# Kernel tuning notes

Hardware: AMD Instinct MI355X
Metric: run time of the kernel (lower is better)

## Reference

```python
import jax, jax.numpy as jnp
import numpy as np

B, S, D, H, DH, DI, K = 2, 2048, 1024, 16, 64, 4096, 3


def layernorm(x, g, b, eps=1e-5):
    m = x.mean(-1, keepdims=True)
    v = ((x - m) ** 2).mean(-1, keepdims=True)
    return (x - m) * jax.lax.rsqrt(v + eps) * g + b


def setup_inputs() -> dict:
    key = jax.random.key(0)
    ks = jax.random.split(key, 8)
    w = lambda k, shape: jax.random.normal(k, shape, jnp.float32) * 0.02
    return dict(
        dec_inp=jax.random.normal(ks[0], (B, S, D), jnp.float32),
        mask=jnp.ones((B, S, 1), dtype=bool),
        Wq=w(ks[1], (D, H * DH)), bq=jnp.zeros((H * DH,), jnp.float32),
        Wk=w(ks[2], (D, H * DH)), bk=jnp.zeros((H * DH,), jnp.float32),
        Wv=w(ks[3], (D, H * DH)), bv=jnp.zeros((H * DH,), jnp.float32),
        Wo=w(ks[4], (H * DH, D)),
        ln1_g=jnp.ones((D,), jnp.float32), ln1_b=jnp.zeros((D,), jnp.float32),
        conv1_w=w(ks[5], (DI, D, K)), conv1_b=jnp.zeros((DI,), jnp.float32),
        conv2_w=w(ks[6], (D, DI, K)), conv2_b=jnp.zeros((D,), jnp.float32),
        ln2_g=jnp.ones((D,), jnp.float32), ln2_b=jnp.zeros((D,), jnp.float32),
    )


def reference(dec_inp, mask, Wq, bq, Wk, bk, Wv, bv, Wo, ln1_g, ln1_b,
              conv1_w, conv1_b, conv2_w, conv2_b, ln2_g, ln2_b):
    scale = 1.0 / np.sqrt(DH)
    x = dec_inp
    pad = ~mask[:, :, 0]  # [B,S] True = masked-out key position (~mask in torch)
    # QKV projections -> [B,H,S,DH]
    q = (x @ Wq + bq).reshape(B, S, H, DH).transpose(0, 2, 1, 3)
    k = (x @ Wk + bk).reshape(B, S, H, DH).transpose(0, 2, 1, 3)
    v = (x @ Wv + bv).reshape(B, S, H, DH).transpose(0, 2, 1, 3)
    scores = jnp.einsum('bhqd,bhkd->bhqk', q, k) * scale  # [B,H,S,S]
    scores = jnp.where(pad[:, None, None, :], jnp.float32(-100000.0), scores)
    p = jax.nn.softmax(scores, axis=-1)
    av = jnp.einsum('bhqk,bhkd->bhqd', p, v)  # [B,H,S,DH]
    # Replicate torch's view quirk: flat (B*H) reinterpreted as (H,B).
    av = av.reshape(B * H, S, DH).reshape(H, B, S, DH).transpose(1, 2, 0, 3).reshape(B, S, H * DH)
    attn_out = av @ Wo  # o_net has no bias
    out = layernorm(x + attn_out, ln1_g, ln1_b)  # post-lnorm (pre_lnorm=False)
    out = out * mask.astype(out.dtype)
    # Conv FFN (non-causal, 'same' padding)
    h = out.transpose(0, 2, 1)  # [B,D,S] NCH
    pd = K // 2
    dn = ('NCH', 'OIH', 'NCH')
    h1 = jax.lax.conv_general_dilated(h, conv1_w, (1,), [(pd, pd)], dimension_numbers=dn)
    h1 = jax.nn.relu(h1 + conv1_b[None, :, None])
    h2 = jax.lax.conv_general_dilated(h1, conv2_w, (1,), [(pd, pd)], dimension_numbers=dn)
    h2 = h2 + conv2_b[None, :, None]
    out2 = layernorm(out + h2.transpose(0, 2, 1), ln2_g, ln2_b)
    return out2 * mask.astype(out2.dtype)
```

## Files before the change

kernel.cpp:

```cpp
#include <hip/hip_runtime.h>


typedef unsigned short u16;
typedef __attribute__((ext_vector_type(8))) short bf16x8;
typedef __attribute__((ext_vector_type(4))) float f32x4;

__device__ __forceinline__ float us2f(u16 u) {
    return __uint_as_float(((unsigned int)u) << 16);
}
__device__ __forceinline__ u16 f2us(float f) {
    unsigned int i = __float_as_uint(f);
    return (u16)((i + 0x7fffu + ((i >> 16) & 1u)) >> 16);
}
__device__ __forceinline__ f32x4 mfma16(bf16x8 a, bf16x8 b, f32x4 c) {
    return __builtin_amdgcn_mfma_f32_16x16x32_bf16(a, b, c, 0, 0, 0);
}
__device__ __forceinline__ void gld16(const u16* g, u16* l) {
    __builtin_amdgcn_global_load_lds(
        (const __attribute__((address_space(1))) unsigned int*)g,
        (__attribute__((address_space(3))) unsigned int*)l, 16, 0, 0);
}

__global__ __launch_bounds__(64)
void sniff_kernel(const u16* __restrict__ w, int* __restrict__ flag) {
    int t = threadIdx.x;
    u16 v = w[2 * t];
    int e = (v >> 7) & 0xFF;
    int ok = (e >= 100 && e <= 140) ? 1 : 0;
    unsigned long long m = __ballot(ok);
    if (t == 0) *flag = (__popcll(m) < 32) ? 1 : 0;
}

__global__ __launch_bounds__(256)
void cvt_x(const void* __restrict__ src, u16* __restrict__ dst,
           const int* __restrict__ flagp) {
    int idx = (blockIdx.x * 256 + threadIdx.x) * 4;
    if (*flagp) {
        float4 f = *(const float4*)((const float*)src + idx);
        u16 o[4] = {f2us(f.x), f2us(f.y), f2us(f.z), f2us(f.w)};
        *(uint2*)(dst + idx) = *(uint2*)o;
    } else {
        *(uint2*)(dst + idx) = *(const uint2*)((const u16*)src + idx);
    }
}

__global__ __launch_bounds__(256)
void cvt_res(const u16* __restrict__ src, float* __restrict__ dst) {
    int idx = (blockIdx.x * 256 + threadIdx.x) * 4;
    u16 s[4];
    *(uint2*)s = *(const uint2*)(src + idx);
    float4 o = {us2f(s[0]), us2f(s[1]), us2f(s[2]), us2f(s[3])};
    *(float4*)(dst + idx) = o;
}

struct Params9 {
    const void* s[9];
    int n[9];
    int off[9];
};
__global__ __launch_bounds__(256)
void cvt_params(Params9 p, u16* __restrict__ base, const int* __restrict__ flagp) {
    int f = *flagp;
    for (int j = 0; j < 9; ++j) {
        const void* s = p.s[j];
        u16* d = base + p.off[j];
        for (int i = threadIdx.x; i < p.n[j]; i += 256)
            d[i] = f ? f2us(((const float*)s)[i]) : ((const u16*)s)[i];
    }
}

__global__ __launch_bounds__(256)
void transpose4f(const void* s0, const void* s1, const void* s2, const void* s3,
                 u16* __restrict__ d0, u16* __restrict__ d1,
                 u16* __restrict__ d2, u16* __restrict__ d3,
                 const int* __restrict__ flagp) {
    const void* src; u16* dst;
    switch (blockIdx.z) {
        case 0: src = s0; dst = d0; break;
        case 1: src = s1; dst = d1; break;
        case 2: src = s2; dst = d2; break;
        default: src = s3; dst = d3; break;
    }
    int f = *flagp;
    __shared__ u16 tl[32][33];
    int tx = threadIdx.x & 31, ty = threadIdx.x >> 5;
    int xc = blockIdx.x * 32 + tx;
#pragma unroll
    for (int r = 0; r < 4; ++r) {
        int yr = blockIdx.y * 32 + ty + r * 8;
        size_t ix = (size_t)yr * 1024 + xc;
        tl[ty + r * 8][tx] = f ? f2us(((const float*)src)[ix]) : ((const u16*)src)[ix];
    }
    __syncthreads();
    int xc2 = blockIdx.y * 32 + tx;
#pragma unroll
    for (int r = 0; r < 4; ++r) {
        int yr2 = blockIdx.x * 32 + ty + r * 8;
        dst[(size_t)yr2 * 1024 + xc2] = tl[tx][ty + r * 8];
    }
}

__global__ __launch_bounds__(256)
void vtrans(const u16* __restrict__ vb, u16* __restrict__ vtg) {
    __shared__ u16 tl[32][33];
    const int st = blockIdx.x, dt = blockIdx.y, bh = blockIdx.z;
    const int b = bh >> 4, h = bh & 15;
    int tx = threadIdx.x & 31, ty = threadIdx.x >> 5;
#pragma unroll
    for (int r = 0; r < 4; ++r) {
        int s = st * 32 + ty + r * 8;
        tl[ty + r * 8][tx] = vb[(size_t)(b * 2048 + s) * 1024 + h * 64 + dt * 32 + tx];
    }
    __syncthreads();
#pragma unroll
    for (int r = 0; r < 4; ++r) {
        int dh = dt * 32 + ty + r * 8;
        vtg[((size_t)bh * 64 + dh) * 2048 + st * 32 + tx] = tl[tx][ty + r * 8];
    }
}

__global__ __launch_bounds__(256)
void deint3g(const void* __restrict__ src, u16* __restrict__ dst,
             size_t eoff, int rs, int c8b, size_t tstr,
             const int* __restrict__ flagp) {
    int idx = blockIdx.x * 256 + threadIdx.x;
    int row = idx >> c8b;
    int c8 = idx & ((1 << c8b) - 1);
    int C = 8 << c8b;
    u16 e[24];
    if (*flagp) {
        const float* sp = (const float*)src + eoff + (size_t)row * rs + (size_t)c8 * 24;
        float tf[24];
#pragma unroll
        for (int i = 0; i < 6; ++i) *(float4*)(tf + i * 4) = *(const float4*)(sp + i * 4);
#pragma unroll
        for (int i = 0; i < 24; ++i) e[i] = f2us(tf[i]);
    } else {
        const u16* sp = (const u16*)src + eoff + (size_t)row * rs + (size_t)c8 * 24;
        *(uint4*)(e + 0)  = *(const uint4*)(sp + 0);
        *(uint4*)(e + 8)  = *(const uint4*)(sp + 8);
        *(uint4*)(e + 16) = *(const uint4*)(sp + 16);
    }
#pragma unroll
    for (int t = 0; t < 3; ++t) {
        u16 o[8];
#pragma unroll
        for (int i = 0; i < 8; ++i) o[i] = e[i * 3 + t];
        *(uint4*)(dst + (size_t)t * tstr + (size_t)row * C + c8 * 8) = *(uint4*)o;
    }
}

__global__ __launch_bounds__(256)
void zero_pads(u16* o1p, u16* h1p, int hN) {
    const int rows[4] = {0, 2049, 2050, 4099};
#pragma unroll
    for (int ri = 0; ri < 4; ++ri) {
        size_t ro = (size_t)rows[ri];
        for (int i = blockIdx.x * 256 + threadIdx.x; i < 1024; i += 256 * gridDim.x)
            o1p[ro * 1024 + i] = 0;
        for (int i = blockIdx.x * 256 + threadIdx.x; i < hN; i += 256 * gridDim.x)
            h1p[ro * (size_t)hN + i] = 0;
    }
}

template <int MODE, bool SHIFT, bool ZSPLIT>
__global__ __launch_bounds__(256)
void gemm_bt(const u16* __restrict__ A, const u16* __restrict__ BT,
             const u16* __restrict__ bias, void* outp,
             int Kc, int Kstr, int N) {
    __shared__ u16 As[128 * 32];
    __shared__ u16 Bs[128 * 32];
    const int tid = threadIdx.x;
    const int lane = tid & 63;
    const int wv = tid >> 6;
    const int wm = (wv >> 1) * 64;
    const int wn = (wv & 1) * 64;
    const int quad = lane >> 4;
    const int l16 = lane & 15;
    const int row0 = blockIdx.y * 128;
    const int col0 = blockIdx.x * 128;
    const int z = ZSPLIT ? blockIdx.z : 0;
    const int lr = lane >> 2;
    const int lc = (lane & 3) * 8;
    const size_t NKf = (size_t)N * Kstr;
    const int tb = row0 >> 11, srow = row0 & 2047;
    const int koff = (ZSPLIT && !SHIFT) ? z * Kc : 0;

    f32x4 acc[4][4];
#pragma unroll
    for (int i = 0; i < 4; ++i)
#pragma unroll
        for (int j = 0; j < 4; ++j) acc[i][j] = {0.f, 0.f, 0.f, 0.f};

    const int nkb = (SHIFT && !ZSPLIT) ? (3 * Kc) >> 5 : Kc >> 5;
    for (int kb = 0; kb < nkb; ++kb) {
        const int kk0 = kb << 5;
        int t, c0;
        if (SHIFT && !ZSPLIT) {
            t = (kk0 >= Kc) + (kk0 >= 2 * Kc);
            c0 = kk0 - t * Kc;
        } else {
            t = (SHIFT && ZSPLIT) ? z : 0;
            c0 = kk0;
        }
        const long arow0 = SHIFT ? (long)tb * 2050 + 1 + srow + t - 1 : (long)row0;
        const u16* Ab = A + (size_t)arow0 * Kstr + koff + c0 + lc;
        const u16* Bb = BT + (size_t)t * NKf + (size_t)col0 * Kstr + koff + c0 + lc;
        __syncthreads();
#pragma unroll
        for (int i = 0; i < 2; ++i) {
            const int rr = wv * 32 + i * 16;
            gld16(Ab + (size_t)(rr + lr) * Kstr, &As[rr * 32]);
            gld16(Bb + (size_t)(rr + lr) * Kstr, &Bs[rr * 32]);
        }
        __syncthreads();

        bf16x8 af[4], bf[4];
#pragma unroll
        for (int i = 0; i < 4; ++i) af[i] = *(const bf16x8*)&As[(wm + i * 16 + l16) * 32 + quad * 8];
#pragma unroll
        for (int j = 0; j < 4; ++j) bf[j] = *(const bf16x8*)&Bs[(wn + j * 16 + l16) * 32 + quad * 8];
#pragma unroll
        for (int i = 0; i < 4; ++i)
#pragma unroll
            for (int j = 0; j < 4; ++j) acc[i][j] = mfma16(af[i], bf[j], acc[i][j]);
    }

#pragma unroll
    for (int i = 0; i < 4; ++i) {
#pragma unroll
        for (int j = 0; j < 4; ++j) {
#pragma unroll
            for (int rg = 0; rg < 4; ++rg) {
                int row = row0 + wm + i * 16 + quad * 4 + rg;
                int col = col0 + wn + j * 16 + l16;
                float v = acc[i][j][rg];
                if (MODE == 2) {
                    size_t orow = (size_t)(row >> 11) * 2050 + 1 + (row & 2047);
                    v = fmaxf(v + us2f(bias[col]), 0.f);
                    ((u16*)outp)[orow * N + col] = f2us(v);
                } else if (MODE == 5) {
                    v += us2f(bias[col]);
                    ((u16*)outp)[(size_t)(col >> 10) * 4194304 + (size_t)row * 1024 + (col & 1023)] = f2us(v);
                } else {
                    unsafeAtomicAdd(&((float*)outp)[(size_t)row * N + col], v);
                }
            }
        }
    }
}

template <int MODE, bool SHIFT>
__global__ __launch_bounds__(512, 4)
void gemm256(const u16* __restrict__ A, const u16* __restrict__ BT,
             const u16* __restrict__ bias, void* __restrict__ outp,
             int sliceK, int kshift, int N, int NT) {
    __shared__ u16 S[3][12288];
    const int tid = threadIdx.x;
    const int lane = tid & 63;
    const int wv = tid >> 6;
    const int wr = wv >> 1;
    const int wc = wv & 1;
    const int quad = lane >> 4;
    const int l16 = lane & 15;
    const int lr = lane >> 2;
    const int lkg = (((lane & 3) ^ ((lane >> 5) << 1)) << 3);
    const int xoff = (quad * 8) ^ ((l16 & 8) << 1);

    int bx, by, bz;
    if (MODE == 5) {
        const int lin = blockIdx.x + 24 * blockIdx.y;
        const int c = lin & 7, j = lin >> 3;
        bx = (c & 3) * 6 + j % 6;
        by = (c >> 2) * 8 + j / 6;
        bz = 0;
    } else if (MODE == 2) {
        const int lin = blockIdx.x + 32 * blockIdx.y;
        const int c = lin & 7, j = lin >> 3;
        bx = (c & 3) * 8 + (j & 7);
        by = (c >> 2) * 8 + (j >> 3);
        bz = 0;
    } else {
        const int lin = blockIdx.x + 8 * blockIdx.y + 128 * blockIdx.z;
        const int c = lin & 7, j = lin >> 3;
        bz = c >> 1;
        by = (c & 1) * 8 + (j >> 3);
        bx = j & 7;
    }
    const int row0 = by * 256;
    const int col0 = bx * 128;
    const int Kstr = 1 << kshift;
    const int z = bz;
    const int tb = row0 >> 11, srow = row0 & 2047;
    const size_t NKf = (size_t)N << kshift;

    f32x4 acc[4][4];
#pragma unroll
    for (int i = 0; i < 4; ++i)
#pragma unroll
        for (int j = 0; j < 4; ++j) acc[i][j] = {0.f, 0.f, 0.f, 0.f};

    auto stage = [&](int kt, int buf) {
        const int kk = z * sliceK + kt * 32;
        const int t = SHIFT ? (kk >> kshift) : 0;
        const int c0 = SHIFT ? (kk & (Kstr - 1)) : kk;
        const long arow0 = SHIFT ? ((long)tb * 2050 + srow + t) : (long)row0;
        const u16* Ab = A + (((size_t)arow0) << kshift) + c0 + lkg;
        const u16* Bb = BT + (SHIFT ? (size_t)t * NKf : (size_t)0)
                           + (((size_t)col0) << kshift) + c0 + lkg;
        u16* SA = S[buf];
        u16* SB = S[buf] + 8192;
#pragma unroll
        for (int j = 0; j < 2; ++j) {
            const int u = wv * 2 + j;
            gld16(Ab + (((size_t)(u * 16 + lr)) << kshift), SA + u * 512);
        }
        gld16(Bb + (((size_t)(wv * 16 + lr)) << kshift), SB + wv * 512);
    };

    auto compute = [&](int buf) {
        const u16* SA = S[buf];
        const u16* SB = S[buf] + 8192;
        bf16x8 af[4], bfr[4];
#pragma unroll
        for (int i = 0; i < 4; ++i)
            af[i] = *(const bf16x8*)&SA[(wr * 64 + i * 16 + l16) * 32 + xoff];
#pragma unroll
        for (int j = 0; j < 4; ++j)
            bfr[j] = *(const bf16x8*)&SB[(wc * 64 + j * 16 + l16) * 32 + xoff];
#pragma unroll
        for (int i = 0; i < 4; ++i)
#pragma unroll
            for (int j = 0; j < 4; ++j) acc[i][j] = mfma16(af[i], bfr[j], acc[i][j]);
    };

    stage(0, 0);
    stage(1, 1);
    for (int kt = 0; kt < NT; ++kt) {
        if (kt + 2 < NT) stage(kt + 2, (kt + 2) % 3);
        __builtin_amdgcn_sched_barrier(0);
        if (kt + 2 < NT)       asm volatile("s_waitcnt vmcnt(6)" ::: "memory");
        else if (kt + 1 < NT)  asm volatile("s_waitcnt vmcnt(3)" ::: "memory");
        else                   asm volatile("s_waitcnt vmcnt(0)" ::: "memory");
        __builtin_amdgcn_s_barrier();
        __builtin_amdgcn_sched_barrier(0);
        compute(kt % 3);
        __builtin_amdgcn_sched_barrier(0);
        asm volatile("s_waitcnt lgkmcnt(0)" ::: "memory");
        __builtin_amdgcn_s_barrier();
    }

#pragma unroll
    for (int i = 0; i < 4; ++i) {
        const int rowb = row0 + wr * 64 + i * 16 + quad * 4;
#pragma unroll
        for (int j = 0; j < 4; ++j) {
            const int col = col0 + wc * 64 + j * 16 + l16;
#pragma unroll
            for (int rg = 0; rg < 4; ++rg) {
                const int row = rowb + rg;
                float v = acc[i][j][rg];
                if (MODE == 2) {
                    size_t orow = (size_t)(row >> 11) * 2050 + 1 + (row & 2047);
                    v = fmaxf(v + us2f(bias[col]), 0.f);
                    ((u16*)outp)[orow * N + col] = f2us(v);
                } else if (MODE == 5) {
                    v += us2f(bias[col]);
                    ((u16*)outp)[(size_t)(col >> 10) * 4194304 + (size_t)row * 1024 + (col & 1023)] = f2us(v);
                } else {
                    unsafeAtomicAdd(&((float*)outp)[(size_t)row * N + col], v);
                }
            }
        }
    }
}

__global__ __launch_bounds__(512)
void attn_kernel(const u16* __restrict__ q, const u16* __restrict__ k,
                 const u16* __restrict__ vtg, u16* __restrict__ av) {
    __shared__ __align__(16) u16 Kt[2][64 * 64];
    __shared__ __align__(16) u16 Vt[2][64 * 64];
    __shared__ __align__(16) u16 P[8][16 * 72];

    const int tid = threadIdx.x;
    const int lane = tid & 63;
    const int w = tid >> 6;
    const int quad = lane >> 4;
    const int l16 = lane & 15;
    const int lin = blockIdx.y * 16 + blockIdx.x;
    const int sw = (lin & 7) * 64 + (lin >> 3);
    const int qt = sw & 15;
    const int bh = sw >> 4;
    const int b = bh >> 4, h = bh & 15;

    const int qrow = b * 2048 + qt * 128 + w * 16 + l16;
    bf16x8 qf[2];
#pragma unroll
    for (int kk = 0; kk < 2; ++kk) {
        const u16* qp = q + ((size_t)qrow * 1024 + h * 64 + kk * 32 + quad * 8);
        u16 tmp[8];
        *(uint4*)tmp = *(const uint4*)qp;
#pragma unroll
        for (int j = 0; j < 8; ++j) tmp[j] = f2us(us2f(tmp[j]) * 0.125f);
        qf[kk] = *(bf16x8*)tmp;
    }

    f32x4 oacc[4];
#pragma unroll
    for (int on = 0; on < 4; ++on) oacc[on] = {0.f, 0.f, 0.f, 0.f};
    float lsum = 0.f;

    const int kr = tid >> 3, kc = tid & 7;
    const u16* kbase = k + (size_t)(b * 2048) * 1024 + h * 64 + kc * 8;
    const u16* vbase = vtg + ((size_t)bh * 64 + kr) * 2048 + kc * 8;
    const int sto = kr * 64 + (((kc) ^ (kr & 7)) << 3);

    const int kg0 = ((quad ^ (l16 & 7)) << 3);
    const int kg1 = (((4 + quad) ^ (l16 & 7)) << 3);

    uint4 kreg, vreg;
    kreg = *(const uint4*)(kbase + (size_t)kr * 1024);
    vreg = *(const uint4*)(vbase);
    *(uint4*)&Kt[0][sto] = kreg;
    *(uint4*)&Vt[0][sto] = vreg;
    kreg = *(const uint4*)(kbase + (size_t)(64 + kr) * 1024);
    vreg = *(const uint4*)(vbase + 64);
    asm volatile("s_waitcnt lgkmcnt(0)" ::: "memory");
    __builtin_amdgcn_s_barrier();

    u16* Pw = P[w];
    for (int kt = 0; kt < 32; ++kt) {
        const int buf = kt & 1;
        if (kt < 31) {
            *(uint4*)&Kt[buf ^ 1][sto] = kreg;
            *(uint4*)&Vt[buf ^ 1][sto] = vreg;
        }
        if (kt < 30) {
            kreg = *(const uint4*)(kbase + (size_t)((kt + 2) * 64 + kr) * 1024);
            vreg = *(const uint4*)(vbase + (kt + 2) * 64);
        }

        f32x4 s[4];
        __builtin_amdgcn_s_setprio(1);
#pragma unroll
        for (int j = 0; j < 4; ++j) {
            const int rb = (j * 16 + l16) * 64;
            bf16x8 kf0 = *(const bf16x8*)&Kt[buf][rb + kg0];
            bf16x8 kf1 = *(const bf16x8*)&Kt[buf][rb + kg1];
            f32x4 z = {0.f, 0.f, 0.f, 0.f};
            z = mfma16(kf0, qf[0], z);
            z = mfma16(kf1, qf[1], z);
            s[j] = z;
        }
        __builtin_amdgcn_s_setprio(0);

#pragma unroll
        for (int j = 0; j < 4; ++j)
#pragma unroll
            for (int r2 = 0; r2 < 4; ++r2) {
                float p = __expf(fminf(s[j][r2], 30.f));
                s[j][r2] = p;
                lsum += p;
            }

#pragma unroll
        for (int j = 0; j < 4; ++j) {
            unsigned int lo, hi;
            asm("v_cvt_pk_bf16_f32 %0, %1, %2" : "=v"(lo) : "v"(s[j][0]), "v"(s[j][1]));
            asm("v_cvt_pk_bf16_f32 %0, %1, %2" : "=v"(hi) : "v"(s[j][2]), "v"(s[j][3]));
            uint2 pk = {lo, hi};
            *(uint2*)&Pw[l16 * 72 + j * 16 + quad * 4] = pk;
        }
        asm volatile("s_waitcnt lgkmcnt(0)" ::: "memory");
        __builtin_amdgcn_sched_barrier(0);

        __builtin_amdgcn_s_setprio(1);
#pragma unroll
        for (int ks = 0; ks < 2; ++ks) {
            bf16x8 pf = *(const bf16x8*)&Pw[l16 * 72 + ks * 32 + quad * 8];
#pragma unroll
            for (int on = 0; on < 4; ++on) {
                bf16x8 vf = *(const bf16x8*)&Vt[buf][(on * 16 + l16) * 64 +
                                                    (((ks * 4 + quad) ^ (l16 & 7)) << 3)];
                oacc[on] = mfma16(vf, pf, oacc[on]);
            }
        }
        __builtin_amdgcn_s_setprio(0);

        asm volatile("s_waitcnt lgkmcnt(0)" ::: "memory");
        __builtin_amdgcn_s_barrier();
    }

    lsum += __shfl_xor(lsum, 16, 64);
    lsum += __shfl_xor(lsum, 32, 64);
    const float inv = 1.f / lsum;

    const int b2 = h & 1, h2 = b * 8 + (h >> 1);
    const size_t obase = (size_t)(b2 * 2048 + qt * 128 + w * 16 + l16) * 1024 + h2 * 64;
#pragma unroll
    for (int on = 0; on < 4; ++on) {
        u16 o[4];
#pragma unroll
        for (int rg = 0; rg < 4; ++rg) o[rg] = f2us(oacc[on][rg] * inv);
        *(uint2*)&av[obase + on * 16 + quad * 4] = *(uint2*)o;
    }
}

template <bool OPAD, bool FINAL, bool PRE2>
__global__ __launch_bounds__(256)
void ln_kernel(const float* __restrict__ in, const u16* __restrict__ g,
               const u16* __restrict__ bb, void* __restrict__ out,
               float* __restrict__ out2, const u16* __restrict__ addv,
               const int* __restrict__ flagp) {
    __shared__ float red[8];
    const int tid = threadIdx.x;
    const int row = blockIdx.x;
    float4 x = *(const float4*)(in + (size_t)row * 1024 + tid * 4);
    float sm = x.x + x.y + x.z + x.w;
#pragma unroll
    for (int msk = 1; msk < 64; msk <<= 1) sm += __shfl_xor(sm, msk, 64);
    if ((tid & 63) == 0) red[tid >> 6] = sm;
    __syncthreads();
    float mean = (red[0] + red[1] + red[2] + red[3]) * (1.f / 1024.f);
    float d0 = x.x - mean, d1 = x.y - mean, d2 = x.z - mean, d3 = x.w - mean;
    float sq = d0 * d0 + d1 * d1 + d2 * d2 + d3 * d3;
#pragma unroll
    for (int msk = 1; msk < 64; msk <<= 1) sq += __shfl_xor(sq, msk, 64);
    if ((tid & 63) == 0) red[4 + (tid >> 6)] = sq;
    __syncthreads();
    float var = (red[4] + red[5] + red[6] + red[7]) * (1.f / 1024.f);
    float rs = rsqrtf(var + 1e-5f);
    int c = tid * 4;
    float v0 = d0 * rs * us2f(g[c + 0]) + us2f(bb[c + 0]);
    float v1 = d1 * rs * us2f(g[c + 1]) + us2f(bb[c + 1]);
    float v2 = d2 * rs * us2f(g[c + 2]) + us2f(bb[c + 2]);
    float v3 = d3 * rs * us2f(g[c + 3]) + us2f(bb[c + 3]);
    size_t orow = OPAD ? ((size_t)(row >> 11) * 2050 + 1 + (row & 2047)) : (size_t)row;
    if (FINAL && *flagp) {
        float4 o = {v0, v1, v2, v3};
        *(float4*)((float*)out + orow * 1024 + c) = o;
    } else {
        u16 o[4] = {f2us(v0), f2us(v1), f2us(v2), f2us(v3)};
        *(uint2*)((u16*)out + orow * 1024 + c) = *(uint2*)o;
    }
    if (PRE2) {
        float4 o2 = {v0 + us2f(addv[c + 0]), v1 + us2f(addv[c + 1]),
                     v2 + us2f(addv[c + 2]), v3 + us2f(addv[c + 3])};
        *(float4*)(out2 + (size_t)row * 1024 + c) = o2;
    }
}


extern "C" void kernel_launch(void* const* d_in, const int* in_sizes, int n_in,
                              void* d_out, int out_size, void* d_ws, size_t ws_size,
                              hipStream_t stream) {
    (void)in_sizes; (void)n_in; (void)out_size;
    const void* x_r   = d_in[0];
    const void* Wq_r  = d_in[2];
    const void* bq_r  = d_in[3];
    const void* Wk_r  = d_in[4];
    const void* bk_r  = d_in[5];
    const void* Wv_r  = d_in[6];
    const void* bv_r  = d_in[7];
    const void* Wo_r  = d_in[8];
    const void* g1_r  = d_in[9];
    const void* b1_r  = d_in[10];
    const void* w1_r  = d_in[11];
    const void* cb1_r = d_in[12];
    const void* w2_r  = d_in[13];
    const void* cb2_r = d_in[14];
    const void* g2_r  = d_in[15];
    const void* b2_r  = d_in[16];

    char* ws = (char*)d_ws;
    #define MB(x) ((size_t)(x) << 20)
    u16*   prm  = (u16*)(ws);
    int*   flag = (int*)(ws + 65536);
    u16*   xcb  = (u16*)(ws + MB(1));
    u16*   qkv  = (u16*)(ws + MB(9));
    u16*   qb   = qkv;
    u16*   kbuf = (u16*)(ws + MB(17));
    u16*   vb   = (u16*)(ws + MB(25));
    u16*   vtg  = (u16*)(ws + MB(33));
    u16*   av   = (u16*)(ws + MB(41));
    u16*   wqkvT= (u16*)(ws + MB(49));
    u16*   woT  = (u16*)(ws + MB(55));
    float* pre  = (float*)(ws + MB(9));
    u16*   o1p  = (u16*)(ws + MB(25));
    const bool full = ws_size >= MB(124);
    u16 *w1t, *w2t, *h1p, *wtc;
    if (full) {
        w1t = (u16*)(ws + MB(41));
        h1p = (u16*)(ws + MB(65));
        w2t = (u16*)(ws + MB(99));
        wtc = nullptr;
    } else {
        wtc = (u16*)(ws + MB(41));
        h1p = (u16*)(ws + MB(47));
        w1t = w2t = nullptr;
    }

    const int O_bq = 0, O_cb1 = 3072, O_cb2 = 7168,
              O_g1 = 8192, O_b1 = 9216, O_g2 = 10240, O_b2 = 11264;

    sniff_kernel<<<1, 64, 0, stream>>>((const u16*)Wq_r, flag);
    Params9 p;
    p.s[0] = bq_r;  p.n[0] = 1024; p.off[0] = 0;
    p.s[1] = bk_r;  p.n[1] = 1024; p.off[1] = 1024;
    p.s[2] = bv_r;  p.n[2] = 1024; p.off[2] = 2048;
    p.s[3] = cb1_r; p.n[3] = 4096; p.off[3] = O_cb1;
    p.s[4] = cb2_r; p.n[4] = 1024; p.off[4] = O_cb2;
    p.s[5] = g1_r;  p.n[5] = 1024; p.off[5] = O_g1;
    p.s[6] = b1_r;  p.n[6] = 1024; p.off[6] = O_b1;
    p.s[7] = g2_r;  p.n[7] = 1024; p.off[7] = O_g2;
    p.s[8] = b2_r;  p.n[8] = 1024; p.off[8] = O_b2;
    cvt_params<<<1, 256, 0, stream>>>(p, prm, flag);
    cvt_x<<<4096, 256, 0, stream>>>(x_r, xcb, flag);
    transpose4f<<<dim3(32, 32, 4), 256, 0, stream>>>(
        Wq_r, Wk_r, Wv_r, Wo_r,
        wqkvT, wqkvT + 1048576, wqkvT + 2097152, woT, flag);

    gemm256<5, false><<<dim3(24, 16), 512, 0, stream>>>(
        xcb, wqkvT, prm + O_bq, qkv, 1024, 10, 3072, 32);
    vtrans<<<dim3(64, 2, 32), 256, 0, stream>>>(vb, vtg);
    attn_kernel<<<dim3(16, 32), 512, 0, stream>>>(qb, kbuf, vtg, av);

    cvt_res<<<4096, 256, 0, stream>>>(xcb, pre);
    gemm_bt<6, false, true><<<dim3(8, 32, 2), 256, 0, stream>>>(
        av, woT, nullptr, pre, 512, 1024, 1024);

    ln_kernel<true, false, true><<<4096, 256, 0, stream>>>(
        pre, prm + O_g1, prm + O_b1, o1p, pre, prm + O_cb2, flag);
    zero_pads<<<16, 256, 0, stream>>>(o1p, h1p, full ? 4096 : 1024);

    if (full) {
        deint3g<<<2048, 256, 0, stream>>>(w1_r, w1t, 0, 3072, 7, 4194304, flag);
        gemm256<2, true><<<dim3(32, 16), 512, 0, stream>>>(
            o1p, w1t, prm + O_cb1, h1p, 3072, 10, 4096, 96);
        deint3g<<<2048, 256, 0, stream>>>(w2_r, w2t, 0, 12288, 9, 4194304, flag);
        gemm256<6, true><<<dim3(8, 16, 4), 512, 0, stream>>>(
            h1p, w2t, nullptr, pre, 3072, 12, 1024, 96);
    } else {
        for (int c = 0; c < 4; ++c) {
            deint3g<<<512, 256, 0, stream>>>(w1_r, wtc, (size_t)c * 1024 * 3072, 3072, 7, 1048576, flag);
            gemm_bt<2, true, false><<<dim3(8, 32), 256, 0, stream>>>(
                o1p, wtc, prm + O_cb1 + c * 1024, h1p, 1024, 1024, 1024);
            deint3g<<<512, 256, 0, stream>>>(w2_r, wtc, (size_t)c * 3072, 12288, 7, 1048576, flag);
            gemm_bt<6, true, true><<<dim3(8, 32, 3), 256, 0, stream>>>(
                h1p, wtc, nullptr, pre, 1024, 1024, 1024);
        }
    }

    ln_kernel<false, true, false><<<4096, 256, 0, stream>>>(
        pre, prm + O_g2, prm + O_b2, d_out, nullptr, nullptr, flag);
}
```

Before: 604.8 us.

## Interleave global-to-LDS prefetch with MFMA halves and raise wave priority

Restructures the GEMM main loop so the prefetch loads for tile kt+2 are issued in pieces between the two halves of the MFMA block, not all at once before the barrier. The wait count is relaxed to vmcnt(3) so only the next tile must be resident. The MFMA bursts are wrapped in s_setprio to favour matrix issue. The aim is to hide global-load issue latency and better overlap memory with compute in the triple-buffered pipeline. It risks changing register pressure and compiler scheduling, since the sched_barriers around compute are removed.

```diff
diff --git a/kernel.cpp b/kernel.cpp
--- a/kernel.cpp
+++ b/kernel.cpp
@@ -300,51 +300,71 @@
 #pragma unroll
         for (int j = 0; j < 4; ++j) acc[i][j] = {0.f, 0.f, 0.f, 0.f};
 
-    auto stage = [&](int kt, int buf) {
+    auto addrs = [&](int kt, const u16** Abp, const u16** Bbp) {
         const int kk = z * sliceK + kt * 32;
         const int t = SHIFT ? (kk >> kshift) : 0;
         const int c0 = SHIFT ? (kk & (Kstr - 1)) : kk;
         const long arow0 = SHIFT ? ((long)tb * 2050 + srow + t) : (long)row0;
-        const u16* Ab = A + (((size_t)arow0) << kshift) + c0 + lkg;
-        const u16* Bb = BT + (SHIFT ? (size_t)t * NKf : (size_t)0)
-                           + (((size_t)col0) << kshift) + c0 + lkg;
-        u16* SA = S[buf];
-        u16* SB = S[buf] + 8192;
-#pragma unroll
-        for (int j = 0; j < 2; ++j) {
-            const int u = wv * 2 + j;
-            gld16(Ab + (((size_t)(u * 16 + lr)) << kshift), SA + u * 512);
-        }
-        gld16(Bb + (((size_t)(wv * 16 + lr)) << kshift), SB + wv * 512);
+        *Abp = A + (((size_t)arow0) << kshift) + c0 + lkg;
+        *Bbp = BT + (SHIFT ? (size_t)t * NKf : (size_t)0)
+                  + (((size_t)col0) << kshift) + c0 + lkg;
     };
-
-    auto compute = [&](int buf) {
+    auto stageA = [&](const u16* Ab, int buf, int j) {
+        const int u = wv * 2 + j;
+        gld16(Ab + (((size_t)(u * 16 + lr)) << kshift), S[buf] + u * 512);
+    };
+    auto stageB = [&](const u16* Bb, int buf) {
+        gld16(Bb + (((size_t)(wv * 16 + lr)) << kshift), S[buf] + 8192 + wv * 512);
+    };
+
+    {
+        const u16 *Ab, *Bb;
+        addrs(0, &Ab, &Bb);
+        stageA(Ab, 0, 0); stageA(Ab, 0, 1); stageB(Bb, 0);
+        addrs(1, &Ab, &Bb);
+        stageA(Ab, 1, 0); stageA(Ab, 1, 1); stageB(Bb, 1);
+    }
+
+    for (int kt = 0; kt < NT; ++kt) {
+        if (kt + 1 < NT) asm volatile("s_waitcnt vmcnt(3)" ::: "memory");
+        else             asm volatile("s_waitcnt vmcnt(0)" ::: "memory");
+        __builtin_amdgcn_s_barrier();
+
+        const int buf = kt % 3;
         const u16* SA = S[buf];
         const u16* SB = S[buf] + 8192;
-        bf16x8 af[4], bfr[4];
-#pragma unroll
-        for (int i = 0; i < 4; ++i)
-            af[i] = *(const bf16x8*)&SA[(wr * 64 + i * 16 + l16) * 32 + xoff];
-#pragma unroll
-        for (int j = 0; j < 4; ++j)
-            bfr[j] = *(const bf16x8*)&SB[(wc * 64 + j * 16 + l16) * 32 + xoff];
-#pragma unroll
-        for (int i = 0; i < 4; ++i)
-#pragma unroll
-            for (int j = 0; j < 4; ++j) acc[i][j] = mfma16(af[i], bfr[j], acc[i][j]);
-    };
-
-    stage(0, 0);
-    stage(1, 1);
-    for (int kt = 0; kt < NT; ++kt) {
-        if (kt + 2 < NT) stage(kt + 2, (kt + 2) % 3);
-        __builtin_amdgcn_sched_barrier(0);
-        if (kt + 2 < NT)       asm volatile("s_waitcnt vmcnt(6)" ::: "memory");
-        else if (kt + 1 < NT)  asm volatile("s_waitcnt vmcnt(3)" ::: "memory");
-        else                   asm volatile("s_waitcnt vmcnt(0)" ::: "memory");
-        __builtin_amdgcn_s_barrier();
-        __builtin_amdgcn_sched_barrier(0);
-        compute(kt % 3);
+        const bool pf = (kt + 2 < NT);
+        const int nb = (kt + 2) % 3;
+        const u16 *Ab = nullptr, *Bb = nullptr;
+        if (pf) addrs(kt + 2, &Ab, &Bb);
+
+        bf16x8 bfr[4];
+#pragma unroll
+        for (int j2 = 0; j2 < 4; ++j2)
+            bfr[j2] = *(const bf16x8*)&SB[(wc * 64 + j2 * 16 + l16) * 32 + xoff];
+
+        if (pf) stageA(Ab, nb, 0);
+        bf16x8 af0 = *(const bf16x8*)&SA[(wr * 64 + 0 * 16 + l16) * 32 + xoff];
+        bf16x8 af1 = *(const bf16x8*)&SA[(wr * 64 + 1 * 16 + l16) * 32 + xoff];
+        __builtin_amdgcn_s_setprio(1);
+#pragma unroll
+        for (int j2 = 0; j2 < 4; ++j2) {
+            acc[0][j2] = mfma16(af0, bfr[j2], acc[0][j2]);
+            acc[1][j2] = mfma16(af1, bfr[j2], acc[1][j2]);
+        }
+        __builtin_amdgcn_s_setprio(0);
+
+        if (pf) { stageA(Ab, nb, 1); stageB(Bb, nb); }
+        bf16x8 af2 = *(const bf16x8*)&SA[(wr * 64 + 2 * 16 + l16) * 32 + xoff];
+        bf16x8 af3 = *(const bf16x8*)&SA[(wr * 64 + 3 * 16 + l16) * 32 + xoff];
+        __builtin_amdgcn_s_setprio(1);
+#pragma unroll
+        for (int j2 = 0; j2 < 4; ++j2) {
+            acc[2][j2] = mfma16(af2, bfr[j2], acc[2][j2]);
+            acc[3][j2] = mfma16(af3, bfr[j2], acc[3][j2]);
+        }
+        __builtin_amdgcn_s_setprio(0);
+
         __builtin_amdgcn_sched_barrier(0);
         asm volatile("s_waitcnt lgkmcnt(0)" ::: "memory");
         __builtin_amdgcn_s_barrier();
```

Measured after the change: 607.6 us. No clear change (+0.5%).
